# Kernel optimization log

Hardware: AMD Instinct MI355X
Metric: run time of the kernel (lower is better)

The kernel has to match this reference:

```python
import jax, jax.numpy as jnp
import numpy as np

D_MODEL = 1024
N_HEADS = 16
D_K = D_MODEL // N_HEADS


def setup_inputs() -> dict:
    key = jax.random.key(0)
    ks = jax.random.split(key, 7)
    B, S = 2, 2048
    q = jax.random.normal(ks[0], (B, S, D_MODEL), dtype=jnp.float32)
    k = jax.random.normal(ks[1], (B, S, D_MODEL), dtype=jnp.float32)
    v = jax.random.normal(ks[2], (B, S, D_MODEL), dtype=jnp.float32)
    mask = jnp.ones((B, 1, S, S), dtype=bool)
    scale = 1.0 / np.sqrt(D_MODEL)
    w_q = jax.random.normal(ks[3], (D_MODEL, D_MODEL), dtype=jnp.float32) * scale
    w_k = jax.random.normal(ks[4], (D_MODEL, D_MODEL), dtype=jnp.float32) * scale
    w_v = jax.random.normal(ks[5], (D_MODEL, D_MODEL), dtype=jnp.float32) * scale
    w_o = jax.random.normal(ks[6], (D_MODEL, D_MODEL), dtype=jnp.float32) * scale
    return {"q": q, "k": k, "v": v, "mask": mask,
            "w_q": w_q, "w_k": w_k, "w_v": w_v, "w_o": w_o}


def reference(q, k, v, mask, w_q, w_k, w_v, w_o):
    B, S, _ = q.shape
    # projections (nn.Linear: x @ W^T, no bias)
    def split_heads(x):  # [B,S,D] -> [B,H,S,d_k]
        return x.reshape(B, -1, N_HEADS, D_K).transpose(0, 2, 1, 3)
    query = split_heads(q @ w_q.T)
    key_h = split_heads(k @ w_k.T)
    value = split_heads(v @ w_v.T)
    # naive scaled dot-product attention: full [B,H,S,S] scores materialized
    scores = jnp.einsum('bhqd,bhkd->bhqk', query, key_h) / jnp.sqrt(
        jnp.asarray(D_K, query.dtype))
    scores = jnp.where(mask, scores, jnp.asarray(-1e9, scores.dtype))
    attn = jax.nn.softmax(scores, axis=-1)  # dropout p=0.0 -> identity
    x = jnp.einsum('bhqk,bhkd->bhqd', attn, value)
    x = x.transpose(0, 2, 1, 3).reshape(B, S, N_HEADS * D_K)
    return x @ w_o.T
```

## Files before the change

### kernel.cpp

```cpp
#include <hip/hip_runtime.h>
#include <hip/hip_bf16.h>
#include <math.h>

typedef __bf16 bf16;
typedef __bf16 bf16x8 __attribute__((ext_vector_type(8)));
typedef float f32x4 __attribute__((ext_vector_type(4)));

#define MFMA16(a, b, c) __builtin_amdgcn_mfma_f32_16x16x32_bf16((a), (b), (c), 0, 0, 0)

__device__ __forceinline__ void gl_lds16(const void* g, void* l) {
    __builtin_amdgcn_global_load_lds(
        (__attribute__((address_space(1))) void*)(g),
        (__attribute__((address_space(3))) void*)(l),
        16, 0, 0);
}

__global__ __launch_bounds__(256) void cvt7(
    const float* __restrict__ w0, const float* __restrict__ w1,
    const float* __restrict__ w2, const float* __restrict__ w3,
    const float* __restrict__ x0, const float* __restrict__ x1,
    const float* __restrict__ x2, bf16* __restrict__ dst) {
    const int z = blockIdx.y;
    const float* src;
    bf16* out;
    if (z < 4) {
        if (blockIdx.x >= 512) return;
        src = (z == 0) ? w0 : (z == 1) ? w1 : (z == 2) ? w2 : w3;
        out = dst + (size_t)z * 1048576;
    } else {
        src = (z == 4) ? x0 : (z == 5) ? x1 : x2;
        out = dst + 4 * 1048576 + (size_t)(z - 4) * 4194304;
    }
    const int i = (blockIdx.x * 256 + threadIdx.x) * 8;
    float4 a = ((const float4*)(src + i))[0];
    float4 b = ((const float4*)(src + i))[1];
    bf16x8 o;
    o[0] = (bf16)a.x; o[1] = (bf16)a.y; o[2] = (bf16)a.z; o[3] = (bf16)a.w;
    o[4] = (bf16)b.x; o[5] = (bf16)b.y; o[6] = (bf16)b.z; o[7] = (bf16)b.w;
    *(bf16x8*)(out + i) = o;
}

template <int EP>
__device__ __forceinline__ void gemm_bf(const bf16* __restrict__ A,
                                        const bf16* __restrict__ B,
                                        void* __restrict__ Cv,
                                        const int m0, const int n0) {
    constexpr int K = 1024;
    __shared__ __align__(16) bf16 As[128 * 32];
    __shared__ __align__(16) bf16 Bs[128 * 32];

    const int t = threadIdx.x;
    const int lane = t & 63;
    const int w = t >> 6;
    const int wm = (w & 1) * 64;
    const int wn = (w >> 1) * 64;
    const int lr = lane & 15;
    const int lq8 = (lane >> 4) * 8;
    const int rq = (lane >> 4) * 4;

    f32x4 acc[4][4] = {};

    const int srow = t >> 2;
    const int sch = (t & 3) * 8;
    char* lA = (char*)As;
    char* lB = (char*)Bs;

    for (int k0 = 0; k0 < K; k0 += 32) {
        gl_lds16(A + (size_t)(m0 + srow) * K + k0 + sch,      lA + t * 16);
        gl_lds16(A + (size_t)(m0 + 64 + srow) * K + k0 + sch, lA + 4096 + t * 16);
        gl_lds16(B + (size_t)(n0 + srow) * K + k0 + sch,      lB + t * 16);
        gl_lds16(B + (size_t)(n0 + 64 + srow) * K + k0 + sch, lB + 4096 + t * 16);
        __syncthreads();

        bf16x8 af[4], bfr[4];
#pragma unroll
        for (int i = 0; i < 4; ++i) {
            af[i]  = *(const bf16x8*)&As[(wm + i * 16 + lr) * 32 + lq8];
            bfr[i] = *(const bf16x8*)&Bs[(wn + i * 16 + lr) * 32 + lq8];
        }
#pragma unroll
        for (int mi = 0; mi < 4; ++mi)
#pragma unroll
            for (int ni = 0; ni < 4; ++ni)
                acc[mi][ni] = MFMA16(af[mi], bfr[ni], acc[mi][ni]);
        __syncthreads();
    }

#pragma unroll
    for (int mi = 0; mi < 4; ++mi) {
#pragma unroll
        for (int ni = 0; ni < 4; ++ni) {
#pragma unroll
            for (int r = 0; r < 4; ++r) {
                const int m = m0 + wm + mi * 16 + rq + r;
                const int n = n0 + wn + ni * 16 + lr;
                const float vv = acc[mi][ni][r];
                if constexpr (EP == 0) {
                    bf16* C = (bf16*)Cv;
                    const int b = m >> 11, s = m & 2047;
                    const int h = n >> 6,  d = n & 63;
                    C[(((size_t)(b * 16 + h)) * 2048 + s) * 64 + d] = (bf16)vv;
                } else if constexpr (EP == 1) {
                    float* C = (float*)Cv;
                    C[(size_t)m * 1024 + n] = vv;
                } else {
                    bf16* C = (bf16*)Cv;
                    C[((size_t)(n >> 11) * 1024 + m) * 2048 + (n & 2047)] = (bf16)vv;
                }
            }
        }
    }
}

__global__ __launch_bounds__(256, 3) void qkv_bf(
    const bf16* __restrict__ Xq, const bf16* __restrict__ Xk,
    const bf16* __restrict__ Xv, const bf16* __restrict__ Wc,
    bf16* __restrict__ Qb, bf16* __restrict__ Kb, bf16* __restrict__ Vb) {
    const int z = blockIdx.z;
    if (z == 0)
        gemm_bf<0>(Xq, Wc, Qb, blockIdx.x * 128, blockIdx.y * 128);
    else if (z == 1)
        gemm_bf<0>(Xk, Wc + 1048576, Kb, blockIdx.x * 128, blockIdx.y * 128);
    else
        gemm_bf<2>(Wc + 2 * 1048576, Xv, Vb, blockIdx.y * 128, blockIdx.x * 128);
}

__global__ __launch_bounds__(256, 2) void out_gemm(
    const bf16* __restrict__ X, const bf16* __restrict__ W, float* __restrict__ C) {
    gemm_bf<1>(X, W, C, blockIdx.x * 128, blockIdx.y * 128);
}

template <int MODE>
__device__ __forceinline__ void gemm_f32tok(const void* __restrict__ Av,
                                            const void* __restrict__ Bv,
                                            bf16* __restrict__ C,
                                            const int m0, const int n0) {
    constexpr int K = 1024;
    __shared__ __align__(16) bf16 As[128 * 32];
    __shared__ __align__(16) bf16 Bs[128 * 32];

    const int t = threadIdx.x;
    const int lane = t & 63;
    const int w = t >> 6;
    const int wm = (w & 1) * 64;
    const int wn = (w >> 1) * 64;
    const int lr = lane & 15;
    const int lq8 = (lane >> 4) * 8;
    const int rq = (lane >> 4) * 4;

    f32x4 acc[4][4] = {};
    const int srow = t >> 2;
    const int sch = (t & 3) * 8;
    const int ar = t >> 1;
    const int ac = (t & 1) * 16;
    char* lA = (char*)As;
    char* lB = (char*)Bs;

    for (int k0 = 0; k0 < K; k0 += 32) {
        if constexpr (MODE == 0) {
            const float* X = (const float*)Av;
            const float* p = X + (size_t)(m0 + ar) * K + k0 + ac;
            float4 f0 = ((const float4*)p)[0], f1 = ((const float4*)p)[1];
            float4 f2 = ((const float4*)p)[2], f3 = ((const float4*)p)[3];
            bf16x8 o0, o1;
            o0[0]=(bf16)f0.x; o0[1]=(bf16)f0.y; o0[2]=(bf16)f0.z; o0[3]=(bf16)f0.w;
            o0[4]=(bf16)f1.x; o0[5]=(bf16)f1.y; o0[6]=(bf16)f1.z; o0[7]=(bf16)f1.w;
            o1[0]=(bf16)f2.x; o1[1]=(bf16)f2.y; o1[2]=(bf16)f2.z; o1[3]=(bf16)f2.w;
            o1[4]=(bf16)f3.x; o1[5]=(bf16)f3.y; o1[6]=(bf16)f3.z; o1[7]=(bf16)f3.w;
            *(bf16x8*)&As[ar * 32 + ac]     = o0;
            *(bf16x8*)&As[ar * 32 + ac + 8] = o1;
        } else {
            const bf16* X = (const bf16*)Av;
            gl_lds16(X + (size_t)(m0 + srow) * K + k0 + sch,      lA + t * 16);
            gl_lds16(X + (size_t)(m0 + 64 + srow) * K + k0 + sch, lA + 4096 + t * 16);
        }
        if constexpr (MODE == 2) {
            const float* X = (const float*)Bv;
            const float* p = X + (size_t)(n0 + ar) * K + k0 + ac;
            float4 f0 = ((const float4*)p)[0], f1 = ((const float4*)p)[1];
            float4 f2 = ((const float4*)p)[2], f3 = ((const float4*)p)[3];
            bf16x8 o0, o1;
            o0[0]=(bf16)f0.x; o0[1]=(bf16)f0.y; o0[2]=(bf16)f0.z; o0[3]=(bf16)f0.w;
            o0[4]=(bf16)f1.x; o0[5]=(bf16)f1.y; o0[6]=(bf16)f1.z; o0[7]=(bf16)f1.w;
            o1[0]=(bf16)f2.x; o1[1]=(bf16)f2.y; o1[2]=(bf16)f2.z; o1[3]=(bf16)f2.w;
            o1[4]=(bf16)f3.x; o1[5]=(bf16)f3.y; o1[6]=(bf16)f3.z; o1[7]=(bf16)f3.w;
            *(bf16x8*)&Bs[ar * 32 + ac]     = o0;
            *(bf16x8*)&Bs[ar * 32 + ac + 8] = o1;
        } else {
            const bf16* W = (const bf16*)Bv;
            gl_lds16(W + (size_t)(n0 + srow) * K + k0 + sch,      lB + t * 16);
            gl_lds16(W + (size_t)(n0 + 64 + srow) * K + k0 + sch, lB + 4096 + t * 16);
        }
        __syncthreads();

        bf16x8 af[4], bfr[4];
#pragma unroll
        for (int i = 0; i < 4; ++i) {
            af[i]  = *(const bf16x8*)&As[(wm + i * 16 + lr) * 32 + lq8];
            bfr[i] = *(const bf16x8*)&Bs[(wn + i * 16 + lr) * 32 + lq8];
        }
#pragma unroll
        for (int mi = 0; mi < 4; ++mi)
#pragma unroll
            for (int ni = 0; ni < 4; ++ni)
                acc[mi][ni] = MFMA16(af[mi], bfr[ni], acc[mi][ni]);
        __syncthreads();
    }

#pragma unroll
    for (int mi = 0; mi < 4; ++mi) {
#pragma unroll
        for (int ni = 0; ni < 4; ++ni) {
#pragma unroll
            for (int r = 0; r < 4; ++r) {
                const int m = m0 + wm + mi * 16 + rq + r;
                const int n = n0 + wn + ni * 16 + lr;
                const float vv = acc[mi][ni][r];
                if constexpr (MODE == 0) {
                    const int b = m >> 11, s = m & 2047;
                    const int h = n >> 6,  d = n & 63;
                    C[(((size_t)(b * 16 + h)) * 2048 + s) * 64 + d] = (bf16)vv;
                } else {
                    C[((size_t)(n >> 11) * 1024 + m) * 2048 + (n & 2047)] = (bf16)vv;
                }
            }
        }
    }
}

__global__ __launch_bounds__(256, 2) void qkv_f32(
    const float* __restrict__ q, const float* __restrict__ k, const float* __restrict__ v,
    const bf16* __restrict__ Wc, bf16* __restrict__ Qb, bf16* __restrict__ Kb,
    bf16* __restrict__ Vb) {
    const int z = blockIdx.z;
    if (z == 0)
        gemm_f32tok<0>(q, Wc, Qb, blockIdx.x * 128, blockIdx.y * 128);
    else if (z == 1)
        gemm_f32tok<0>(k, Wc + 1048576, Kb, blockIdx.x * 128, blockIdx.y * 128);
    else
        gemm_f32tok<2>(Wc + 2 * 1048576, v, Vb, blockIdx.y * 128, blockIdx.x * 128);
}

__global__ __launch_bounds__(256, 4) void attn_kernel(
    const bf16* __restrict__ Qb, const bf16* __restrict__ Kb,
    const bf16* __restrict__ Vb, bf16* __restrict__ Xb) {
    constexpr int S = 2048;

    __shared__ __align__(16) bf16 Qs[64 * 64];
    __shared__ __align__(16) bf16 Ks[64 * 64];
    __shared__ __align__(16) bf16 Ps[64 * 64];
    __shared__ __align__(16) bf16 Vt[80 * 64];

    const int t = threadIdx.x;
    const int lane = t & 63;
    const int w = t >> 6;
    const int lr = lane & 15;
    const int lq8 = (lane >> 4) * 8;
    const int q4 = (lane >> 4) * 4;
    const int bh = blockIdx.y;
    const int q0 = blockIdx.x * 64;
    const bf16* Q  = Qb + (size_t)bh * S * 64;
    const bf16* Kh = Kb + (size_t)bh * S * 64;
    const bf16* Vh = Vb + (size_t)bh * 64 * S;

    const float qscale = 0.125f * 1.4426950408889634f;
#pragma unroll
    for (int p = 0; p < 2; ++p) {
        const int c = p * 256 + t;
        const int row = c >> 3, cc = c & 7;
        bf16x8 vq = *(const bf16x8*)(Q + (size_t)(q0 + row) * 64 + cc * 8);
#pragma unroll
        for (int e = 0; e < 8; ++e) vq[e] = (bf16)((float)vq[e] * qscale);
        *(bf16x8*)&Qs[row * 64 + (cc ^ (row & 7)) * 8] = vq;
    }
    for (int idx = t; idx < 1024; idx += 256) {
        const int r = idx >> 6;
        Vt[(64 + r) * 64 + (idx & 63)] = (r == 0) ? (bf16)1.0f : (bf16)0.0f;
    }

    f32x4 oacc[5] = {};

    const int srow = t >> 2;
    const int scc = (t & 3) * 2;
    bf16x8 pk[2], pv[2];
#pragma unroll
    for (int c = 0; c < 2; ++c) {
        pk[c] = *(const bf16x8*)(Kh + (size_t)srow * 64 + (scc + c) * 8);
        pv[c] = *(const bf16x8*)(Vh + (size_t)srow * S + (scc + c) * 8);
    }

    const int rowA = w * 16 + lr;
    const int swzA = (lr & 7) << 3;
    const int swzP = (((rowA >> 1) & 7)) << 3;

    for (int j = 0; j < S / 64; ++j) {
        __syncthreads();
#pragma unroll
        for (int c = 0; c < 2; ++c) {
            *(bf16x8*)&Ks[srow * 64 + ((scc + c) ^ (srow & 7)) * 8] = pk[c];
            *(bf16x8*)&Vt[srow * 64 + ((scc + c) ^ (srow & 7)) * 8] = pv[c];
        }
        __syncthreads();

        f32x4 sacc[4] = {};
#pragma unroll
        for (int ks = 0; ks < 64; ks += 32) {
            bf16x8 af = *(const bf16x8*)&Qs[rowA * 64 + ((ks + lq8) ^ swzA)];
            bf16x8 bk[4];
#pragma unroll
            for (int nt = 0; nt < 4; ++nt)
                bk[nt] = *(const bf16x8*)&Ks[(nt * 16 + lr) * 64 + ((ks + lq8) ^ swzA)];
#pragma unroll
            for (int nt = 0; nt < 4; ++nt)
                sacc[nt] = MFMA16(af, bk[nt], sacc[nt]);
        }

        if (j + 1 < S / 64) {
            const bf16* Kt = Kh + (size_t)(j + 1) * 64 * 64;
            const bf16* Vg = Vh + (size_t)(j + 1) * 64;
#pragma unroll
            for (int c = 0; c < 2; ++c) {
                pk[c] = *(const bf16x8*)(Kt + (size_t)srow * 64 + (scc + c) * 8);
                pv[c] = *(const bf16x8*)(Vg + (size_t)srow * S + (scc + c) * 8);
            }
        }

#pragma unroll
        for (int r = 0; r < 4; ++r) {
            const int row = w * 16 + q4 + r;
            const int swz = ((row >> 1) & 7) << 3;
#pragma unroll
            for (int nt = 0; nt < 4; ++nt)
                Ps[row * 64 + ((nt * 16 + lr) ^ swz)] =
                    (bf16)exp2f(fminf(sacc[nt][r], 100.f));
        }

#pragma unroll
        for (int ks = 0; ks < 64; ks += 32) {
            bf16x8 ap = *(const bf16x8*)&Ps[rowA * 64 + ((ks + lq8) ^ swzP)];
            bf16x8 bv[5];
#pragma unroll
            for (int nt2 = 0; nt2 < 5; ++nt2)
                bv[nt2] = *(const bf16x8*)&Vt[(nt2 * 16 + lr) * 64 + ((ks + lq8) ^ swzA)];
#pragma unroll
            for (int nt2 = 0; nt2 < 5; ++nt2)
                oacc[nt2] = MFMA16(ap, bv[nt2], oacc[nt2]);
        }
    }

    const int b = bh >> 4, h = bh & 15;
#pragma unroll
    for (int r = 0; r < 4; ++r) {
        const float lv = __shfl(oacc[4][r], lane & 48, 64);
        const float inv = 1.f / fmaxf(lv, 1e-30f);
        const int row = w * 16 + q4 + r;
        const size_t base = ((size_t)(b * 2048 + q0 + row)) * 1024 + h * 64;
#pragma unroll
        for (int nt2 = 0; nt2 < 4; ++nt2)
            Xb[base + nt2 * 16 + lr] = (bf16)(oacc[nt2][r] * inv);
    }
}

extern "C" void kernel_launch(void* const* d_in, const int* in_sizes, int n_in,
                              void* d_out, int out_size, void* d_ws, size_t ws_size,
                              hipStream_t stream) {
    const float* q  = (const float*)d_in[0];
    const float* k  = (const float*)d_in[1];
    const float* v  = (const float*)d_in[2];
    const float* wq = (const float*)d_in[4];
    const float* wk = (const float*)d_in[5];
    const float* wv = (const float*)d_in[6];
    const float* wo = (const float*)d_in[7];
    float* out = (float*)d_out;

    const bool big = ws_size >= (size_t)64 * 1024 * 1024;
    bf16* Wc = (bf16*)d_ws;
    const dim3 blk(256);

    if (big) {
        bf16* Xq = Wc + 4 * 1048576;
        bf16* Xk = Xq + 4194304;
        bf16* Xv = Xk + 4194304;
        bf16* Qb = Xv + 4194304;
        bf16* Kb = Qb + 4194304;
        bf16* Vb = Kb + 4194304;
        bf16* Xb = Vb + 4194304;
        cvt7<<<dim3(2048, 7), blk, 0, stream>>>(wq, wk, wv, wo, q, k, v, Wc);
        qkv_bf<<<dim3(32, 8, 3), blk, 0, stream>>>(Xq, Xk, Xv, Wc, Qb, Kb, Vb);
        attn_kernel<<<dim3(32, 32), blk, 0, stream>>>(Qb, Kb, Vb, Xb);
        out_gemm<<<dim3(32, 8), blk, 0, stream>>>(Xb, Wc + 3 * 1048576, out);
    } else {
        bf16* Qb = Wc + 4 * 1048576;
        bf16* Kb = Qb + 4194304;
        bf16* Vb = Kb + 4194304;
        bf16* Xb = Vb + 4194304;
        cvt7<<<dim3(512, 4), blk, 0, stream>>>(wq, wk, wv, wo, q, k, v, Wc);
        qkv_f32<<<dim3(32, 8, 3), blk, 0, stream>>>(q, k, v, Wc, Qb, Kb, Vb);
        attn_kernel<<<dim3(32, 32), blk, 0, stream>>>(Qb, Kb, Vb, Xb);
        out_gemm<<<dim3(32, 8), blk, 0, stream>>>(Xb, Wc + 3 * 1048576, out);
    }
}
```

Baseline: 256.3 us.

## Enlarge QKV GEMM N-tile to 256 and attention query tile to 128

The QKV projection GEMM now computes a 128x256 output tile per block, with each wave holding 4x8 accumulators, and the grid shrinks to match. The attention kernel processes 128 query rows per block, two 16-row M tiles per wave, so each loaded K/V tile is reused across twice as many queries. This reduces LDS and global traffic per FLOP, at the cost of more registers, lower occupancy (launch bounds lowered to 2) and fewer blocks in flight.

```diff
diff --git a/kernel.cpp b/kernel.cpp
--- a/kernel.cpp
+++ b/kernel.cpp
@@ -40,25 +40,25 @@
     *(bf16x8*)(out + i) = o;
 }
 
-template <int EP>
+template <int EP, int NI>
 __device__ __forceinline__ void gemm_bf(const bf16* __restrict__ A,
                                         const bf16* __restrict__ B,
                                         void* __restrict__ Cv,
                                         const int m0, const int n0) {
     constexpr int K = 1024;
     __shared__ __align__(16) bf16 As[128 * 32];
-    __shared__ __align__(16) bf16 Bs[128 * 32];
+    __shared__ __align__(16) bf16 Bs[NI * 32 * 32];
 
     const int t = threadIdx.x;
     const int lane = t & 63;
     const int w = t >> 6;
     const int wm = (w & 1) * 64;
-    const int wn = (w >> 1) * 64;
+    const int wn = (w >> 1) * (NI * 16);
     const int lr = lane & 15;
     const int lq8 = (lane >> 4) * 8;
     const int rq = (lane >> 4) * 4;
 
-    f32x4 acc[4][4] = {};
+    f32x4 acc[4][NI] = {};
 
     const int srow = t >> 2;
     const int sch = (t & 3) * 8;
@@ -68,20 +68,23 @@
     for (int k0 = 0; k0 < K; k0 += 32) {
         gl_lds16(A + (size_t)(m0 + srow) * K + k0 + sch,      lA + t * 16);
         gl_lds16(A + (size_t)(m0 + 64 + srow) * K + k0 + sch, lA + 4096 + t * 16);
-        gl_lds16(B + (size_t)(n0 + srow) * K + k0 + sch,      lB + t * 16);
-        gl_lds16(B + (size_t)(n0 + 64 + srow) * K + k0 + sch, lB + 4096 + t * 16);
-        __syncthreads();
-
-        bf16x8 af[4], bfr[4];
-#pragma unroll
-        for (int i = 0; i < 4; ++i) {
-            af[i]  = *(const bf16x8*)&As[(wm + i * 16 + lr) * 32 + lq8];
-            bfr[i] = *(const bf16x8*)&Bs[(wn + i * 16 + lr) * 32 + lq8];
-        }
+#pragma unroll
+        for (int bseg = 0; bseg < NI / 2; ++bseg)
+            gl_lds16(B + (size_t)(n0 + bseg * 64 + srow) * K + k0 + sch,
+                     lB + bseg * 4096 + t * 16);
+        __syncthreads();
+
+        bf16x8 af[4], bfr[NI];
+#pragma unroll
+        for (int i = 0; i < 4; ++i)
+            af[i] = *(const bf16x8*)&As[(wm + i * 16 + lr) * 32 + lq8];
+#pragma unroll
+        for (int ni = 0; ni < NI; ++ni)
+            bfr[ni] = *(const bf16x8*)&Bs[(wn + ni * 16 + lr) * 32 + lq8];
 #pragma unroll
         for (int mi = 0; mi < 4; ++mi)
 #pragma unroll
-            for (int ni = 0; ni < 4; ++ni)
+            for (int ni = 0; ni < NI; ++ni)
                 acc[mi][ni] = MFMA16(af[mi], bfr[ni], acc[mi][ni]);
         __syncthreads();
     }
@@ -89,7 +92,7 @@
 #pragma unroll
     for (int mi = 0; mi < 4; ++mi) {
 #pragma unroll
-        for (int ni = 0; ni < 4; ++ni) {
+        for (int ni = 0; ni < NI; ++ni) {
 #pragma unroll
             for (int r = 0; r < 4; ++r) {
                 const int m = m0 + wm + mi * 16 + rq + r;
@@ -112,22 +115,24 @@
     }
 }
 
-__global__ __launch_bounds__(256, 3) void qkv_bf(
+__global__ __launch_bounds__(256, 2) void qkv_bf(
     const bf16* __restrict__ Xq, const bf16* __restrict__ Xk,
     const bf16* __restrict__ Xv, const bf16* __restrict__ Wc,
     bf16* __restrict__ Qb, bf16* __restrict__ Kb, bf16* __restrict__ Vb) {
     const int z = blockIdx.z;
     if (z == 0)
-        gemm_bf<0>(Xq, Wc, Qb, blockIdx.x * 128, blockIdx.y * 128);
+        gemm_bf<0, 8>(Xq, Wc, Qb, blockIdx.x * 128, blockIdx.y * 256);
     else if (z == 1)
-        gemm_bf<0>(Xk, Wc + 1048576, Kb, blockIdx.x * 128, blockIdx.y * 128);
-    else
-        gemm_bf<2>(Wc + 2 * 1048576, Xv, Vb, blockIdx.y * 128, blockIdx.x * 128);
+        gemm_bf<0, 8>(Xk, Wc + 1048576, Kb, blockIdx.x * 128, blockIdx.y * 256);
+    else {
+        const int id = blockIdx.y * 32 + blockIdx.x;
+        gemm_bf<2, 8>(Wc + 2 * 1048576, Xv, Vb, (id & 7) * 128, (id >> 3) * 256);
+    }
 }
 
 __global__ __launch_bounds__(256, 2) void out_gemm(
     const bf16* __restrict__ X, const bf16* __restrict__ W, float* __restrict__ C) {
-    gemm_bf<1>(X, W, C, blockIdx.x * 128, blockIdx.y * 128);
+    gemm_bf<1, 4>(X, W, C, blockIdx.x * 128, blockIdx.y * 128);
 }
 
 template <int MODE>
@@ -241,14 +246,14 @@
         gemm_f32tok<2>(Wc + 2 * 1048576, v, Vb, blockIdx.y * 128, blockIdx.x * 128);
 }
 
-__global__ __launch_bounds__(256, 4) void attn_kernel(
+__global__ __launch_bounds__(256, 2) void attn_kernel(
     const bf16* __restrict__ Qb, const bf16* __restrict__ Kb,
     const bf16* __restrict__ Vb, bf16* __restrict__ Xb) {
     constexpr int S = 2048;
 
-    __shared__ __align__(16) bf16 Qs[64 * 64];
+    __shared__ __align__(16) bf16 Qs[128 * 64];
     __shared__ __align__(16) bf16 Ks[64 * 64];
-    __shared__ __align__(16) bf16 Ps[64 * 64];
+    __shared__ __align__(16) bf16 Ps[128 * 64];
     __shared__ __align__(16) bf16 Vt[80 * 64];
 
     const int t = threadIdx.x;
@@ -258,14 +263,14 @@
     const int lq8 = (lane >> 4) * 8;
     const int q4 = (lane >> 4) * 4;
     const int bh = blockIdx.y;
-    const int q0 = blockIdx.x * 64;
+    const int q0 = blockIdx.x * 128;
     const bf16* Q  = Qb + (size_t)bh * S * 64;
     const bf16* Kh = Kb + (size_t)bh * S * 64;
     const bf16* Vh = Vb + (size_t)bh * 64 * S;
 
     const float qscale = 0.125f * 1.4426950408889634f;
 #pragma unroll
-    for (int p = 0; p < 2; ++p) {
+    for (int p = 0; p < 4; ++p) {
         const int c = p * 256 + t;
         const int row = c >> 3, cc = c & 7;
         bf16x8 vq = *(const bf16x8*)(Q + (size_t)(q0 + row) * 64 + cc * 8);
@@ -278,7 +283,7 @@
         Vt[(64 + r) * 64 + (idx & 63)] = (r == 0) ? (bf16)1.0f : (bf16)0.0f;
     }
 
-    f32x4 oacc[5] = {};
+    f32x4 oacc[2][5] = {};
 
     const int srow = t >> 2;
     const int scc = (t & 3) * 2;
@@ -289,9 +294,8 @@
         pv[c] = *(const bf16x8*)(Vh + (size_t)srow * S + (scc + c) * 8);
     }
 
-    const int rowA = w * 16 + lr;
     const int swzA = (lr & 7) << 3;
-    const int swzP = (((rowA >> 1) & 7)) << 3;
+    const int swzP = ((lr >> 1) & 7) << 3;
 
     for (int j = 0; j < S / 64; ++j) {
         __syncthreads();
@@ -302,17 +306,21 @@
         }
         __syncthreads();
 
-        f32x4 sacc[4] = {};
+        f32x4 sacc[2][4] = {};
 #pragma unroll
         for (int ks = 0; ks < 64; ks += 32) {
-            bf16x8 af = *(const bf16x8*)&Qs[rowA * 64 + ((ks + lq8) ^ swzA)];
-            bf16x8 bk[4];
+            bf16x8 af[2], bk[4];
+#pragma unroll
+            for (int mt = 0; mt < 2; ++mt)
+                af[mt] = *(const bf16x8*)&Qs[(w * 32 + mt * 16 + lr) * 64 + ((ks + lq8) ^ swzA)];
 #pragma unroll
             for (int nt = 0; nt < 4; ++nt)
                 bk[nt] = *(const bf16x8*)&Ks[(nt * 16 + lr) * 64 + ((ks + lq8) ^ swzA)];
 #pragma unroll
-            for (int nt = 0; nt < 4; ++nt)
-                sacc[nt] = MFMA16(af, bk[nt], sacc[nt]);
+            for (int mt = 0; mt < 2; ++mt)
+#pragma unroll
+                for (int nt = 0; nt < 4; ++nt)
+                    sacc[mt][nt] = MFMA16(af[mt], bk[nt], sacc[mt][nt]);
         }
 
         if (j + 1 < S / 64) {
@@ -326,38 +334,48 @@
         }
 
 #pragma unroll
-        for (int r = 0; r < 4; ++r) {
-            const int row = w * 16 + q4 + r;
-            const int swz = ((row >> 1) & 7) << 3;
-#pragma unroll
-            for (int nt = 0; nt < 4; ++nt)
-                Ps[row * 64 + ((nt * 16 + lr) ^ swz)] =
-                    (bf16)exp2f(fminf(sacc[nt][r], 100.f));
+        for (int mt = 0; mt < 2; ++mt) {
+#pragma unroll
+            for (int r = 0; r < 4; ++r) {
+                const int row = w * 32 + mt * 16 + q4 + r;
+                const int swz = ((row >> 1) & 7) << 3;
+#pragma unroll
+                for (int nt = 0; nt < 4; ++nt)
+                    Ps[row * 64 + ((nt * 16 + lr) ^ swz)] =
+                        (bf16)exp2f(fminf(sacc[mt][nt][r], 100.f));
+            }
         }
 
 #pragma unroll
         for (int ks = 0; ks < 64; ks += 32) {
-            bf16x8 ap = *(const bf16x8*)&Ps[rowA * 64 + ((ks + lq8) ^ swzP)];
-            bf16x8 bv[5];
+            bf16x8 ap[2], bv[5];
+#pragma unroll
+            for (int mt = 0; mt < 2; ++mt)
+                ap[mt] = *(const bf16x8*)&Ps[(w * 32 + mt * 16 + lr) * 64 + ((ks + lq8) ^ swzP)];
 #pragma unroll
             for (int nt2 = 0; nt2 < 5; ++nt2)
                 bv[nt2] = *(const bf16x8*)&Vt[(nt2 * 16 + lr) * 64 + ((ks + lq8) ^ swzA)];
 #pragma unroll
-            for (int nt2 = 0; nt2 < 5; ++nt2)
-                oacc[nt2] = MFMA16(ap, bv[nt2], oacc[nt2]);
+            for (int mt = 0; mt < 2; ++mt)
+#pragma unroll
+                for (int nt2 = 0; nt2 < 5; ++nt2)
+                    oacc[mt][nt2] = MFMA16(ap[mt], bv[nt2], oacc[mt][nt2]);
         }
     }
 
     const int b = bh >> 4, h = bh & 15;
 #pragma unroll
-    for (int r = 0; r < 4; ++r) {
-        const float lv = __shfl(oacc[4][r], lane & 48, 64);
-        const float inv = 1.f / fmaxf(lv, 1e-30f);
-        const int row = w * 16 + q4 + r;
-        const size_t base = ((size_t)(b * 2048 + q0 + row)) * 1024 + h * 64;
-#pragma unroll
-        for (int nt2 = 0; nt2 < 4; ++nt2)
-            Xb[base + nt2 * 16 + lr] = (bf16)(oacc[nt2][r] * inv);
+    for (int mt = 0; mt < 2; ++mt) {
+#pragma unroll
+        for (int r = 0; r < 4; ++r) {
+            const float lv = __shfl(oacc[mt][4][r], lane & 48, 64);
+            const float inv = 1.f / fmaxf(lv, 1e-30f);
+            const int row = w * 32 + mt * 16 + q4 + r;
+            const size_t base = ((size_t)(b * 2048 + q0 + row)) * 1024 + h * 64;
+#pragma unroll
+            for (int nt2 = 0; nt2 < 4; ++nt2)
+                Xb[base + nt2 * 16 + lr] = (bf16)(oacc[mt][nt2][r] * inv);
+        }
     }
 }
 
@@ -386,8 +404,8 @@
         bf16* Vb = Kb + 4194304;
         bf16* Xb = Vb + 4194304;
         cvt7<<<dim3(2048, 7), blk, 0, stream>>>(wq, wk, wv, wo, q, k, v, Wc);
-        qkv_bf<<<dim3(32, 8, 3), blk, 0, stream>>>(Xq, Xk, Xv, Wc, Qb, Kb, Vb);
-        attn_kernel<<<dim3(32, 32), blk, 0, stream>>>(Qb, Kb, Vb, Xb);
+        qkv_bf<<<dim3(32, 4, 3), blk, 0, stream>>>(Xq, Xk, Xv, Wc, Qb, Kb, Vb);
+        attn_kernel<<<dim3(16, 32), blk, 0, stream>>>(Qb, Kb, Vb, Xb);
         out_gemm<<<dim3(32, 8), blk, 0, stream>>>(Xb, Wc + 3 * 1048576, out);
     } else {
         bf16* Qb = Wc + 4 * 1048576;
@@ -396,7 +414,7 @@
         bf16* Xb = Vb + 4194304;
         cvt7<<<dim3(512, 4), blk, 0, stream>>>(wq, wk, wv, wo, q, k, v, Wc);
         qkv_f32<<<dim3(32, 8, 3), blk, 0, stream>>>(q, k, v, Wc, Qb, Kb, Vb);
-        attn_kernel<<<dim3(32, 32), blk, 0, stream>>>(Qb, Kb, Vb, Xb);
+        attn_kernel<<<dim3(16, 32), blk, 0, stream>>>(Qb, Kb, Vb, Xb);
         out_gemm<<<dim3(32, 8), blk, 0, stream>>>(Xb, Wc + 3 * 1048576, out);
     }
 }
```

Result: slower. 267.9 us (+4.5%).

## Fold Q scale into weights, coalesce QKV epilogue via LDS, trim attention LDS

Applied to the files above, without the earlier changes.

Folds the softmax scale and log2e into the bf16 conversion of w_q, so the attention kernel loads Q straight into LDS with async global-to-LDS copies and keeps the Q fragments in registers. Q and P now share one LDS buffer, and the ones-row for the row-sum becomes a register constant, which cuts LDS per block. The QKV GEMM epilogue stages its tile through a swizzled LDS buffer and writes 16-byte vectors instead of scattered 2-byte stores. The costs are an extra barrier and LDS pass in the epilogue, and an extra bf16 rounding of the scaled weights.

```diff
diff --git a/kernel.cpp b/kernel.cpp
--- a/kernel.cpp
+++ b/kernel.cpp
@@ -31,12 +31,15 @@
         src = (z == 4) ? x0 : (z == 5) ? x1 : x2;
         out = dst + 4 * 1048576 + (size_t)(z - 4) * 4194304;
     }
+    const float sc = (z == 0) ? 0.125f * 1.4426950408889634f : 1.0f;
     const int i = (blockIdx.x * 256 + threadIdx.x) * 8;
     float4 a = ((const float4*)(src + i))[0];
     float4 b = ((const float4*)(src + i))[1];
     bf16x8 o;
-    o[0] = (bf16)a.x; o[1] = (bf16)a.y; o[2] = (bf16)a.z; o[3] = (bf16)a.w;
-    o[4] = (bf16)b.x; o[5] = (bf16)b.y; o[6] = (bf16)b.z; o[7] = (bf16)b.w;
+    o[0] = (bf16)(a.x * sc); o[1] = (bf16)(a.y * sc);
+    o[2] = (bf16)(a.z * sc); o[3] = (bf16)(a.w * sc);
+    o[4] = (bf16)(b.x * sc); o[5] = (bf16)(b.y * sc);
+    o[6] = (bf16)(b.z * sc); o[7] = (bf16)(b.w * sc);
     *(bf16x8*)(out + i) = o;
 }
 
@@ -46,8 +49,9 @@
                                         void* __restrict__ Cv,
                                         const int m0, const int n0) {
     constexpr int K = 1024;
-    __shared__ __align__(16) bf16 As[128 * 32];
-    __shared__ __align__(16) bf16 Bs[128 * 32];
+    __shared__ __align__(16) bf16 smem[16384];
+    bf16* As = smem;
+    bf16* Bs = smem + 4096;
 
     const int t = threadIdx.x;
     const int lane = t & 63;
@@ -86,29 +90,52 @@
         __syncthreads();
     }
 
-#pragma unroll
-    for (int mi = 0; mi < 4; ++mi) {
-#pragma unroll
-        for (int ni = 0; ni < 4; ++ni) {
-#pragma unroll
-            for (int r = 0; r < 4; ++r) {
-                const int m = m0 + wm + mi * 16 + rq + r;
-                const int n = n0 + wn + ni * 16 + lr;
-                const float vv = acc[mi][ni][r];
+    if constexpr (EP == 1) {
+        float* C = (float*)Cv;
+#pragma unroll
+        for (int mi = 0; mi < 4; ++mi)
+#pragma unroll
+            for (int ni = 0; ni < 4; ++ni)
+#pragma unroll
+                for (int r = 0; r < 4; ++r) {
+                    const int m = m0 + wm + mi * 16 + rq + r;
+                    const int n = n0 + wn + ni * 16 + lr;
+                    C[(size_t)m * 1024 + n] = acc[mi][ni][r];
+                }
+    } else {
+#pragma unroll
+        for (int mi = 0; mi < 4; ++mi)
+#pragma unroll
+            for (int ni = 0; ni < 4; ++ni)
+#pragma unroll
+                for (int r = 0; r < 4; ++r) {
+                    const int row = wm + mi * 16 + rq + r;
+                    const int col = wn + ni * 16 + lr;
+                    const int ch = ((col >> 3) & 8) | (((col >> 3) & 7) ^ (row & 7));
+                    smem[row * 128 + ch * 8 + (col & 7)] = (bf16)acc[mi][ni][r];
+                }
+        __syncthreads();
+        const int cc = t & 7;
+        const int rb = t >> 3;
+        bf16* C = (bf16*)Cv;
+#pragma unroll
+        for (int g = 0; g < 2; ++g)
+#pragma unroll
+            for (int rep = 0; rep < 4; ++rep) {
+                const int row = rep * 32 + rb;
+                const int chunk = g * 8 + cc;
+                const int ch = (chunk & 8) | ((chunk & 7) ^ (row & 7));
+                const bf16x8 vv = *(const bf16x8*)&smem[row * 128 + ch * 8];
                 if constexpr (EP == 0) {
-                    bf16* C = (bf16*)Cv;
-                    const int b = m >> 11, s = m & 2047;
-                    const int h = n >> 6,  d = n & 63;
-                    C[(((size_t)(b * 16 + h)) * 2048 + s) * 64 + d] = (bf16)vv;
-                } else if constexpr (EP == 1) {
-                    float* C = (float*)Cv;
-                    C[(size_t)m * 1024 + n] = vv;
+                    const int tok = m0 + row, feat = n0 + chunk * 8;
+                    const int b = tok >> 11, s = tok & 2047;
+                    const int h = feat >> 6, d = feat & 63;
+                    *(bf16x8*)&C[(((size_t)(b * 16 + h)) * 2048 + s) * 64 + d] = vv;
                 } else {
-                    bf16* C = (bf16*)Cv;
-                    C[((size_t)(n >> 11) * 1024 + m) * 2048 + (n & 2047)] = (bf16)vv;
+                    const int feat = m0 + row, tok = n0 + chunk * 8;
+                    *(bf16x8*)&C[((size_t)(tok >> 11) * 1024 + feat) * 2048 + (tok & 2047)] = vv;
                 }
             }
-        }
     }
 }
 
@@ -246,10 +273,9 @@
     const bf16* __restrict__ Vb, bf16* __restrict__ Xb) {
     constexpr int S = 2048;
 
-    __shared__ __align__(16) bf16 Qs[64 * 64];
+    __shared__ __align__(16) bf16 QPs[64 * 64];
     __shared__ __align__(16) bf16 Ks[64 * 64];
-    __shared__ __align__(16) bf16 Ps[64 * 64];
-    __shared__ __align__(16) bf16 Vt[80 * 64];
+    __shared__ __align__(16) bf16 Vt[64 * 64];
 
     const int t = threadIdx.x;
     const int lane = t & 63;
@@ -263,22 +289,8 @@
     const bf16* Kh = Kb + (size_t)bh * S * 64;
     const bf16* Vh = Vb + (size_t)bh * 64 * S;
 
-    const float qscale = 0.125f * 1.4426950408889634f;
-#pragma unroll
-    for (int p = 0; p < 2; ++p) {
-        const int c = p * 256 + t;
-        const int row = c >> 3, cc = c & 7;
-        bf16x8 vq = *(const bf16x8*)(Q + (size_t)(q0 + row) * 64 + cc * 8);
-#pragma unroll
-        for (int e = 0; e < 8; ++e) vq[e] = (bf16)((float)vq[e] * qscale);
-        *(bf16x8*)&Qs[row * 64 + (cc ^ (row & 7)) * 8] = vq;
-    }
-    for (int idx = t; idx < 1024; idx += 256) {
-        const int r = idx >> 6;
-        Vt[(64 + r) * 64 + (idx & 63)] = (r == 0) ? (bf16)1.0f : (bf16)0.0f;
-    }
-
-    f32x4 oacc[5] = {};
+    gl_lds16(Q + (size_t)q0 * 64 + t * 8,        (char*)QPs + t * 16);
+    gl_lds16(Q + (size_t)q0 * 64 + 2048 + t * 8, (char*)QPs + 4096 + t * 16);
 
     const int srow = t >> 2;
     const int scc = (t & 3) * 2;
@@ -289,9 +301,19 @@
         pv[c] = *(const bf16x8*)(Vh + (size_t)srow * S + (scc + c) * 8);
     }
 
+    bf16x8 onesf;
+#pragma unroll
+    for (int e = 0; e < 8; ++e) onesf[e] = (lr == 0) ? (bf16)1.0f : (bf16)0.0f;
+
+    f32x4 oacc[5] = {};
     const int rowA = w * 16 + lr;
     const int swzA = (lr & 7) << 3;
-    const int swzP = (((rowA >> 1) & 7)) << 3;
+    const int swzP = ((rowA >> 1) & 7) << 3;
+
+    __syncthreads();
+    bf16x8 afr[2];
+    afr[0] = *(const bf16x8*)&QPs[rowA * 64 + lq8];
+    afr[1] = *(const bf16x8*)&QPs[rowA * 64 + 32 + lq8];
 
     for (int j = 0; j < S / 64; ++j) {
         __syncthreads();
@@ -304,15 +326,14 @@
 
         f32x4 sacc[4] = {};
 #pragma unroll
-        for (int ks = 0; ks < 64; ks += 32) {
-            bf16x8 af = *(const bf16x8*)&Qs[rowA * 64 + ((ks + lq8) ^ swzA)];
+        for (int s2 = 0; s2 < 2; ++s2) {
             bf16x8 bk[4];
 #pragma unroll
             for (int nt = 0; nt < 4; ++nt)
-                bk[nt] = *(const bf16x8*)&Ks[(nt * 16 + lr) * 64 + ((ks + lq8) ^ swzA)];
+                bk[nt] = *(const bf16x8*)&Ks[(nt * 16 + lr) * 64 + ((s2 * 32 + lq8) ^ swzA)];
 #pragma unroll
             for (int nt = 0; nt < 4; ++nt)
-                sacc[nt] = MFMA16(af, bk[nt], sacc[nt]);
+                sacc[nt] = MFMA16(afr[s2], bk[nt], sacc[nt]);
         }
 
         if (j + 1 < S / 64) {
@@ -331,20 +352,21 @@
             const int swz = ((row >> 1) & 7) << 3;
 #pragma unroll
             for (int nt = 0; nt < 4; ++nt)
-                Ps[row * 64 + ((nt * 16 + lr) ^ swz)] =
+                QPs[row * 64 + ((nt * 16 + lr) ^ swz)] =
                     (bf16)exp2f(fminf(sacc[nt][r], 100.f));
         }
 
 #pragma unroll
         for (int ks = 0; ks < 64; ks += 32) {
-            bf16x8 ap = *(const bf16x8*)&Ps[rowA * 64 + ((ks + lq8) ^ swzP)];
-            bf16x8 bv[5];
-#pragma unroll
-            for (int nt2 = 0; nt2 < 5; ++nt2)
+            bf16x8 ap = *(const bf16x8*)&QPs[rowA * 64 + ((ks + lq8) ^ swzP)];
+            bf16x8 bv[4];
+#pragma unroll
+            for (int nt2 = 0; nt2 < 4; ++nt2)
                 bv[nt2] = *(const bf16x8*)&Vt[(nt2 * 16 + lr) * 64 + ((ks + lq8) ^ swzA)];
 #pragma unroll
-            for (int nt2 = 0; nt2 < 5; ++nt2)
+            for (int nt2 = 0; nt2 < 4; ++nt2)
                 oacc[nt2] = MFMA16(ap, bv[nt2], oacc[nt2]);
+            oacc[4] = MFMA16(ap, onesf, oacc[4]);
         }
     }
 
```

After: 268.8 us. 1.05x slower.
